# Kernel tuning notes

Measured on AMD Instinct MI355X. Metric: run time of the kernel, lower is better.

## Reference

```python
import jax, jax.numpy as jnp
import numpy as np


def setup_inputs() -> dict:
    key = jax.random.key(0)
    kq, kk, kv = jax.random.split(key, 3)
    B, H, S, D = 4, 16, 1024, 64
    Q = jax.random.normal(kq, (B, H, S, D), dtype=jnp.float32)
    K = jax.random.normal(kk, (B, H, S, D), dtype=jnp.float32)
    V = jax.random.normal(kv, (B, H, S, D), dtype=jnp.float32)
    attn_mask = jnp.ones((B, 1, 1, S), dtype=jnp.int32)  # unused by the original forward
    return {"Q": Q, "K": K, "V": V, "attn_mask": attn_mask, "d_k": D}


def reference(Q, K, V, attn_mask, d_k):
    # scores = Q @ K^T / sqrt(d_k)   -> [B, H, S, S]
    scores = jnp.einsum("bhqd,bhkd->bhqk", Q, K) / jnp.sqrt(jnp.float32(d_k))
    # attn_mask is accepted but never applied in the original module.
    p_attn = jax.nn.softmax(scores, axis=-1)
    out = jnp.einsum("bhqk,bhkd->bhqd", p_attn, V)  # [B, H, S, D]
    return (out, p_attn)
```

## Files before the change

### kernel.cpp

```cpp
#include <hip/hip_runtime.h>
#include <hip/hip_bf16.h>

#define B_N 4
#define H_N 16
#define S_N 1024
#define D_N 64
#define NELEM (B_N * H_N * S_N * D_N)

typedef __bf16 bf16;
typedef bf16  bf16x4 __attribute__((ext_vector_type(4)));
typedef bf16  bf16x8 __attribute__((ext_vector_type(8)));
typedef float f32x4  __attribute__((ext_vector_type(4)));
typedef unsigned int u32x2 __attribute__((ext_vector_type(2)));

#define AS1 __attribute__((address_space(1)))
#define AS3 __attribute__((address_space(3)))
#define GLL16(gp, lp) __builtin_amdgcn_global_load_lds((const AS1 void*)(gp), (AS3 void*)(lp), 16, 0, 0)

__global__ __launch_bounds__(256)
void prep_qk(const float* __restrict__ Q, const float* __restrict__ K,
             bf16* __restrict__ Qb, bf16* __restrict__ Kb)
{
    int t = blockIdx.x * 256 + threadIdx.x;
    const int half = NELEM / 8;
    bool isQ = t < half;
    int tt = isQ ? t : t - half;
    int row = tt >> 3, sub = tt & 7;
    const float* src = (isQ ? Q : K) + (size_t)row * 64 + sub * 8;
    float4 f0 = *(const float4*)src;
    float4 f1 = *(const float4*)(src + 4);
    float s = isQ ? 0.125f : 1.0f;
    bf16x8 o;
    o[0] = (bf16)(f0.x * s); o[1] = (bf16)(f0.y * s);
    o[2] = (bf16)(f0.z * s); o[3] = (bf16)(f0.w * s);
    o[4] = (bf16)(f1.x * s); o[5] = (bf16)(f1.y * s);
    o[6] = (bf16)(f1.z * s); o[7] = (bf16)(f1.w * s);
    int slot = isQ ? sub : (sub ^ (row & 7));
    bf16* dst = (isQ ? Qb : Kb) + (size_t)row * 64 + slot * 8;
    *(bf16x8*)dst = o;
}

__global__ __launch_bounds__(256)
void prep_v(const float* __restrict__ V, bf16* __restrict__ Vt)
{
    int wid  = blockIdx.x * 4 + (threadIdx.x >> 6);
    int lane = threadIdx.x & 63;
    int bh = wid >> 7, chunk = wid & 127;
    const float* src = V + (size_t)bh * S_N * D_N + (size_t)chunk * 8 * 64 + lane;
    bf16x8 o;
#pragma unroll
    for (int j = 0; j < 8; ++j) o[j] = (bf16)src[j * 64];
    int slot = (chunk & 7) ^ (lane & 7);
    bf16* dst = Vt + (size_t)bh * D_N * S_N + (size_t)lane * S_N
                   + (chunk >> 3) * 64 + slot * 8;
    *(bf16x8*)dst = o;
}

__global__ __launch_bounds__(256)
void sdpa_main(const bf16* __restrict__ Qb, const bf16* __restrict__ Kb,
               const bf16* __restrict__ Vt, float* __restrict__ Og,
               float* __restrict__ Pg)
{
    __shared__ __attribute__((aligned(128))) bf16 K_lds[2][4096];
    __shared__ __attribute__((aligned(128))) bf16 V_lds[2][4096];
    __shared__ __attribute__((aligned(128))) bf16 Pt_lds[4][1024];

    const int bid = blockIdx.x;
    const int swz = (bid & 7) * 128 + (bid >> 3);
    const int bh = swz >> 4, qtile = swz & 15;

    const int tid = threadIdx.x;
    const int wave = tid >> 6, lane = tid & 63;
    const int l16 = lane & 15, lgrp = lane >> 4;
    const int swx = (l16 & 7) << 4;

    const bf16* Qp = Qb + (size_t)bh * S_N * D_N;
    const bf16* Kp = Kb + (size_t)bh * S_N * D_N;
    const bf16* Vp = Vt + (size_t)bh * D_N * S_N;
    float* Op = Og + (size_t)bh * S_N * D_N;
    float* Pp = Pg + (size_t)bh * S_N * S_N;

    const int qrow = qtile * 64 + wave * 16 + l16;
    bf16x8 aq[2];
    aq[0] = *(const bf16x8*)(Qp + (size_t)qrow * 64 + lgrp * 8);
    aq[1] = *(const bf16x8*)(Qp + (size_t)qrow * 64 + 32 + lgrp * 8);

    auto stage_k = [&](int kt, int buf) {
        const bf16* gk = Kp + (size_t)kt * 64;
        GLL16(gk + (wave    ) * 512 + lane * 8, &K_lds[buf][(wave    ) * 512]);
        GLL16(gk + (wave + 4) * 512 + lane * 8, &K_lds[buf][(wave + 4) * 512]);
    };
    auto stage_v = [&](int kt, int buf) {
        const int dr = lane >> 3, c7 = lane & 7;
        GLL16(Vp + (size_t)((wave    ) * 8 + dr) * S_N + kt + c7 * 8, &V_lds[buf][(wave    ) * 512]);
        GLL16(Vp + (size_t)((wave + 4) * 8 + dr) * S_N + kt + c7 * 8, &V_lds[buf][(wave + 4) * 512]);
    };

    auto scores = [&](const bf16* base, f32x4 (&acc)[4]) {
#pragma unroll
        for (int kb = 0; kb < 4; ++kb) {
            acc[kb] = (f32x4){0.f, 0.f, 0.f, 0.f};
#pragma unroll
            for (int ds = 0; ds < 2; ++ds) {
                bf16x8 bk = *(const bf16x8*)((const char*)base
                            + (kb * 16 + l16) * 128
                            + ((ds * 64 + lgrp * 16) ^ swx));
                acc[kb] = __builtin_amdgcn_mfma_f32_16x16x32_bf16(aq[ds], bk, acc[kb], 0, 0, 0);
            }
        }
    };

    float lsum[4] = {0.f, 0.f, 0.f, 0.f};
    stage_k(0, 0);
    for (int t = 0; t < 16; ++t) {
        if (t < 15) {
            stage_k((t + 1) * 64, (t + 1) & 1);
            asm volatile("s_waitcnt vmcnt(2)" ::: "memory");
        } else {
            asm volatile("s_waitcnt vmcnt(0)" ::: "memory");
        }
        __builtin_amdgcn_s_barrier();
        f32x4 acc[4];
        scores(&K_lds[t & 1][0], acc);
#pragma unroll
        for (int kb = 0; kb < 4; ++kb)
#pragma unroll
            for (int r = 0; r < 4; ++r) lsum[r] += __expf(acc[kb][r]);
        __builtin_amdgcn_s_barrier();
    }
    float rl[4];
#pragma unroll
    for (int r = 0; r < 4; ++r) {
        float s = lsum[r];
        s += __shfl_xor(s, 1, 64);
        s += __shfl_xor(s, 2, 64);
        s += __shfl_xor(s, 4, 64);
        s += __shfl_xor(s, 8, 64);
        rl[r] = 1.0f / s;
    }

    f32x4 oacc[4];
#pragma unroll
    for (int db = 0; db < 4; ++db) oacc[db] = (f32x4){0.f, 0.f, 0.f, 0.f};

    const unsigned ptoff = (unsigned)(uintptr_t)(AS3 bf16*)(&Pt_lds[wave][0]);
    const int qg = qtile * 64 + wave * 16 + l16;

    stage_k(0, 0);
    stage_v(0, 0);
    for (int t = 0; t < 16; ++t) {
        const int kt = t * 64, buf = t & 1;
        if (t < 15) {
            stage_k(kt + 64, buf ^ 1);
            stage_v(kt + 64, buf ^ 1);
        }
        if (t == 0 || t == 15) asm volatile("s_waitcnt vmcnt(4)" ::: "memory");
        else                   asm volatile("s_waitcnt vmcnt(8)" ::: "memory");
        __builtin_amdgcn_s_barrier();

        f32x4 acc[4];
        scores(&K_lds[buf][0], acc);

#pragma unroll
        for (int kb = 0; kb < 4; ++kb) {
            bf16x4 pk;
#pragma unroll
            for (int r = 0; r < 4; ++r) pk[r] = (bf16)(__expf(acc[kb][r]) * rl[r]);
            *(bf16x4*)((char*)&Pt_lds[wave][0] + (kb * 16 + l16) * 32 + lgrp * 8) = pk;
        }
        asm volatile("s_waitcnt lgkmcnt(0)" ::: "memory");

        const bf16* vb = &V_lds[buf][0];
#pragma unroll
        for (int ks = 0; ks < 2; ++ks) {
            bf16x8 bv0 = *(const bf16x8*)((const char*)vb + (l16     ) * 128 + ((ks * 64 + lgrp * 16) ^ swx));
            bf16x8 bv1 = *(const bf16x8*)((const char*)vb + (16 + l16) * 128 + ((ks * 64 + lgrp * 16) ^ swx));
            bf16x8 bv2 = *(const bf16x8*)((const char*)vb + (32 + l16) * 128 + ((ks * 64 + lgrp * 16) ^ swx));
            bf16x8 bv3 = *(const bf16x8*)((const char*)vb + (48 + l16) * 128 + ((ks * 64 + lgrp * 16) ^ swx));

            u32x2 t0, t1;
            unsigned a = ptoff + ks * 1024 + lgrp * 256 + l16 * 8;
            asm volatile("ds_read_b64_tr_b16 %0, %2\n\t"
                         "ds_read_b64_tr_b16 %1, %2 offset:128"
                         : "=&v"(t0), "=&v"(t1) : "v"(a));
            asm volatile("s_waitcnt lgkmcnt(0)" ::: "memory");
            __builtin_amdgcn_sched_barrier(0);

            bf16x8 ap;
            ((unsigned*)&ap)[0] = t0[0]; ((unsigned*)&ap)[1] = t0[1];
            ((unsigned*)&ap)[2] = t1[0]; ((unsigned*)&ap)[3] = t1[1];

            float4 o0, o1;
            o0.x = __uint_as_float(t0[0] << 16);
            o0.y = __uint_as_float(t0[0] & 0xffff0000u);
            o0.z = __uint_as_float(t0[1] << 16);
            o0.w = __uint_as_float(t0[1] & 0xffff0000u);
            o1.x = __uint_as_float(t1[0] << 16);
            o1.y = __uint_as_float(t1[0] & 0xffff0000u);
            o1.z = __uint_as_float(t1[1] << 16);
            o1.w = __uint_as_float(t1[1] & 0xffff0000u);
            float* pp = Pp + (size_t)qg * S_N + kt + ks * 32 + lgrp * 8;
            *(float4*)pp = o0;
            *(float4*)(pp + 4) = o1;

            oacc[0] = __builtin_amdgcn_mfma_f32_16x16x32_bf16(ap, bv0, oacc[0], 0, 0, 0);
            oacc[1] = __builtin_amdgcn_mfma_f32_16x16x32_bf16(ap, bv1, oacc[1], 0, 0, 0);
            oacc[2] = __builtin_amdgcn_mfma_f32_16x16x32_bf16(ap, bv2, oacc[2], 0, 0, 0);
            oacc[3] = __builtin_amdgcn_mfma_f32_16x16x32_bf16(ap, bv3, oacc[3], 0, 0, 0);
        }
        __builtin_amdgcn_s_barrier();
    }

    const int qb0 = qtile * 64 + wave * 16 + lgrp * 4;
#pragma unroll
    for (int db = 0; db < 4; ++db)
#pragma unroll
        for (int r = 0; r < 4; ++r)
            Op[(size_t)(qb0 + r) * D_N + db * 16 + l16] = oacc[db][r];
}

__global__ __launch_bounds__(256)
void sdpa_fused(const float* __restrict__ Qg, const float* __restrict__ Kg,
                const float* __restrict__ Vg, float* __restrict__ Og,
                float* __restrict__ Pg)
{
    constexpr int LDP = 72;
    __shared__ bf16 K_lds [64][LDP];
    __shared__ bf16 Vt_lds[64][LDP];
    __shared__ bf16 P_lds [4][16][LDP];

    const int qtile = blockIdx.x;
    const int bh    = blockIdx.y;
    const int tid   = threadIdx.x;
    const int wave  = tid >> 6;
    const int lane  = tid & 63;
    const int l16   = lane & 15;
    const int lgrp  = lane >> 4;

    const float* Qp = Qg + (size_t)bh * S_N * D_N;
    const float* Kp = Kg + (size_t)bh * S_N * D_N;
    const float* Vp = Vg + (size_t)bh * S_N * D_N;
    float* Op = Og + (size_t)bh * S_N * D_N;
    float* Pp = Pg + (size_t)bh * S_N * S_N;

    const int qrow = qtile * 64 + wave * 16 + l16;
    bf16x8 aq[2];
#pragma unroll
    for (int ds = 0; ds < 2; ++ds) {
        const float* src = Qp + qrow * D_N + ds * 32 + lgrp * 8;
        float4 f0 = *(const float4*)(src);
        float4 f1 = *(const float4*)(src + 4);
        aq[ds][0] = (bf16)(f0.x * 0.125f); aq[ds][1] = (bf16)(f0.y * 0.125f);
        aq[ds][2] = (bf16)(f0.z * 0.125f); aq[ds][3] = (bf16)(f0.w * 0.125f);
        aq[ds][4] = (bf16)(f1.x * 0.125f); aq[ds][5] = (bf16)(f1.y * 0.125f);
        aq[ds][6] = (bf16)(f1.z * 0.125f); aq[ds][7] = (bf16)(f1.w * 0.125f);
    }

    auto stage_k = [&](int kt) {
#pragma unroll
        for (int i = 0; i < 4; ++i) {
            int slot = tid + i * 256;
            int row = slot >> 4, c4 = slot & 15;
            float4 f = *(const float4*)(Kp + (kt + row) * D_N + c4 * 4);
            bf16x4 pk = {(bf16)f.x, (bf16)f.y, (bf16)f.z, (bf16)f.w};
            *(bf16x4*)&K_lds[row][c4 * 4] = pk;
        }
    };
    auto stage_v = [&](int kt) {
#pragma unroll
        for (int i = 0; i < 4; ++i) {
            int slot = tid + i * 256;
            int row = slot >> 4, c4 = slot & 15;
            float4 f = *(const float4*)(Vp + (kt + row) * D_N + c4 * 4);
            Vt_lds[c4 * 4 + 0][row] = (bf16)f.x;
            Vt_lds[c4 * 4 + 1][row] = (bf16)f.y;
            Vt_lds[c4 * 4 + 2][row] = (bf16)f.z;
            Vt_lds[c4 * 4 + 3][row] = (bf16)f.w;
        }
    };
    auto compute_scores = [&](f32x4 (&acc)[4]) {
#pragma unroll
        for (int kb = 0; kb < 4; ++kb) {
            acc[kb] = (f32x4){0.f, 0.f, 0.f, 0.f};
#pragma unroll
            for (int ds = 0; ds < 2; ++ds) {
                bf16x8 bk = *(const bf16x8*)&K_lds[kb * 16 + l16][ds * 32 + lgrp * 8];
                acc[kb] = __builtin_amdgcn_mfma_f32_16x16x32_bf16(aq[ds], bk, acc[kb], 0, 0, 0);
            }
        }
    };

    float lsum[4] = {0.f, 0.f, 0.f, 0.f};
    for (int kt = 0; kt < S_N; kt += 64) {
        __syncthreads();
        stage_k(kt);
        __syncthreads();
        f32x4 acc[4];
        compute_scores(acc);
#pragma unroll
        for (int kb = 0; kb < 4; ++kb)
#pragma unroll
            for (int r = 0; r < 4; ++r) lsum[r] += __expf(acc[kb][r]);
    }
    float rl[4];
#pragma unroll
    for (int r = 0; r < 4; ++r) {
        float s = lsum[r];
        s += __shfl_xor(s, 1, 64);
        s += __shfl_xor(s, 2, 64);
        s += __shfl_xor(s, 4, 64);
        s += __shfl_xor(s, 8, 64);
        rl[r] = 1.0f / s;
    }

    f32x4 oacc[4];
#pragma unroll
    for (int db = 0; db < 4; ++db) oacc[db] = (f32x4){0.f, 0.f, 0.f, 0.f};
    const int qb0 = qtile * 64 + wave * 16 + lgrp * 4;

    for (int kt = 0; kt < S_N; kt += 64) {
        __syncthreads();
        stage_k(kt);
        stage_v(kt);
        __syncthreads();

        f32x4 acc[4];
        compute_scores(acc);
#pragma unroll
        for (int kb = 0; kb < 4; ++kb) {
#pragma unroll
            for (int r = 0; r < 4; ++r) {
                float p = __expf(acc[kb][r]) * rl[r];
                Pp[(size_t)(qb0 + r) * S_N + (kt + kb * 16 + l16)] = p;
                P_lds[wave][lgrp * 4 + r][kb * 16 + l16] = (bf16)p;
            }
        }
#pragma unroll
        for (int ks = 0; ks < 2; ++ks) {
            bf16x8 ap = *(const bf16x8*)&P_lds[wave][l16][ks * 32 + lgrp * 8];
#pragma unroll
            for (int db = 0; db < 4; ++db) {
                bf16x8 bv = *(const bf16x8*)&Vt_lds[db * 16 + l16][ks * 32 + lgrp * 8];
                oacc[db] = __builtin_amdgcn_mfma_f32_16x16x32_bf16(ap, bv, oacc[db], 0, 0, 0);
            }
        }
    }

#pragma unroll
    for (int db = 0; db < 4; ++db)
#pragma unroll
        for (int r = 0; r < 4; ++r)
            Op[(size_t)(qb0 + r) * D_N + db * 16 + l16] = oacc[db][r];
}

extern "C" void kernel_launch(void* const* d_in, const int* in_sizes, int n_in,
                              void* d_out, int out_size, void* d_ws, size_t ws_size,
                              hipStream_t stream) {
    const float* Q = (const float*)d_in[0];
    const float* K = (const float*)d_in[1];
    const float* V = (const float*)d_in[2];
    float* Out = (float*)d_out;
    float* P   = (float*)d_out + (size_t)NELEM;

    const size_t need = (size_t)NELEM * 2 * 3;
    if (ws_size >= need) {
        bf16* Qb = (bf16*)d_ws;
        bf16* Kb = Qb + NELEM;
        bf16* Vt = Kb + NELEM;
        prep_qk<<<dim3(2 * NELEM / 8 / 256), dim3(256), 0, stream>>>(Q, K, Qb, Kb);
        prep_v<<<dim3(64 * 128 / 4), dim3(256), 0, stream>>>(V, Vt);
        sdpa_main<<<dim3(1024), dim3(256), 0, stream>>>(Qb, Kb, Vt, Out, P);
    } else {
        sdpa_fused<<<dim3(16, 64), dim3(256), 0, stream>>>(Q, K, V, Out, P);
    }
}
```

Measured before the change: 105.1 us.

## Merge K/V prep kernels, convert Q in-kernel, reuse V LDS for wider K staging

Drops the separate Q bf16 conversion: the main kernel now loads fp32 Q rows, scales them and converts them into registers. The K and V prep kernels become a single launch. The first (row-sum) pass now processes 128 keys per step, borrowing the V LDS buffers as a second double buffer for K. The second pass issues the next tile's loads after the score MFMAs and uses __syncthreads instead of explicit vmcnt waits, which trades fine-grained overlap for simpler synchronization.

```diff
diff --git a/kernel.cpp b/kernel.cpp
--- a/kernel.cpp
+++ b/kernel.cpp
@@ -18,46 +18,38 @@
 #define GLL16(gp, lp) __builtin_amdgcn_global_load_lds((const AS1 void*)(gp), (AS3 void*)(lp), 16, 0, 0)
 
 __global__ __launch_bounds__(256)
-void prep_qk(const float* __restrict__ Q, const float* __restrict__ K,
-             bf16* __restrict__ Qb, bf16* __restrict__ Kb)
+void prep_kv(const float* __restrict__ K, const float* __restrict__ V,
+             bf16* __restrict__ Kb, bf16* __restrict__ Vt)
 {
-    int t = blockIdx.x * 256 + threadIdx.x;
-    const int half = NELEM / 8;
-    bool isQ = t < half;
-    int tt = isQ ? t : t - half;
-    int row = tt >> 3, sub = tt & 7;
-    const float* src = (isQ ? Q : K) + (size_t)row * 64 + sub * 8;
-    float4 f0 = *(const float4*)src;
-    float4 f1 = *(const float4*)(src + 4);
-    float s = isQ ? 0.125f : 1.0f;
-    bf16x8 o;
-    o[0] = (bf16)(f0.x * s); o[1] = (bf16)(f0.y * s);
-    o[2] = (bf16)(f0.z * s); o[3] = (bf16)(f0.w * s);
-    o[4] = (bf16)(f1.x * s); o[5] = (bf16)(f1.y * s);
-    o[6] = (bf16)(f1.z * s); o[7] = (bf16)(f1.w * s);
-    int slot = isQ ? sub : (sub ^ (row & 7));
-    bf16* dst = (isQ ? Qb : Kb) + (size_t)row * 64 + slot * 8;
-    *(bf16x8*)dst = o;
+    const int b = blockIdx.x;
+    if (b < 2048) {
+        int t = b * 256 + threadIdx.x;
+        int row = t >> 3, sub = t & 7;
+        const float* src = K + (size_t)row * 64 + sub * 8;
+        float4 f0 = *(const float4*)src;
+        float4 f1 = *(const float4*)(src + 4);
+        bf16x8 o;
+        o[0] = (bf16)f0.x; o[1] = (bf16)f0.y; o[2] = (bf16)f0.z; o[3] = (bf16)f0.w;
+        o[4] = (bf16)f1.x; o[5] = (bf16)f1.y; o[6] = (bf16)f1.z; o[7] = (bf16)f1.w;
+        int slot = sub ^ (row & 7);
+        *(bf16x8*)(Kb + (size_t)row * 64 + slot * 8) = o;
+    } else {
+        int wid  = (b - 2048) * 4 + (threadIdx.x >> 6);
+        int lane = threadIdx.x & 63;
+        int bh = wid >> 7, chunk = wid & 127;
+        const float* src = V + (size_t)bh * S_N * D_N + (size_t)chunk * 8 * 64 + lane;
+        bf16x8 o;
+#pragma unroll
+        for (int j = 0; j < 8; ++j) o[j] = (bf16)src[j * 64];
+        int slot = (chunk & 7) ^ (lane & 7);
+        bf16* dst = Vt + (size_t)bh * D_N * S_N + (size_t)lane * S_N
+                       + (chunk >> 3) * 64 + slot * 8;
+        *(bf16x8*)dst = o;
+    }
 }
 
 __global__ __launch_bounds__(256)
-void prep_v(const float* __restrict__ V, bf16* __restrict__ Vt)
-{
-    int wid  = blockIdx.x * 4 + (threadIdx.x >> 6);
-    int lane = threadIdx.x & 63;
-    int bh = wid >> 7, chunk = wid & 127;
-    const float* src = V + (size_t)bh * S_N * D_N + (size_t)chunk * 8 * 64 + lane;
-    bf16x8 o;
-#pragma unroll
-    for (int j = 0; j < 8; ++j) o[j] = (bf16)src[j * 64];
-    int slot = (chunk & 7) ^ (lane & 7);
-    bf16* dst = Vt + (size_t)bh * D_N * S_N + (size_t)lane * S_N
-                   + (chunk >> 3) * 64 + slot * 8;
-    *(bf16x8*)dst = o;
-}
-
-__global__ __launch_bounds__(256)
-void sdpa_main(const bf16* __restrict__ Qb, const bf16* __restrict__ Kb,
+void sdpa_main(const float* __restrict__ Qf, const bf16* __restrict__ Kb,
                const bf16* __restrict__ Vt, float* __restrict__ Og,
                float* __restrict__ Pg)
 {
@@ -74,7 +66,7 @@
     const int l16 = lane & 15, lgrp = lane >> 4;
     const int swx = (l16 & 7) << 4;
 
-    const bf16* Qp = Qb + (size_t)bh * S_N * D_N;
+    const float* Qp = Qf + (size_t)bh * S_N * D_N;
     const bf16* Kp = Kb + (size_t)bh * S_N * D_N;
     const bf16* Vp = Vt + (size_t)bh * D_N * S_N;
     float* Op = Og + (size_t)bh * S_N * D_N;
@@ -82,18 +74,33 @@
 
     const int qrow = qtile * 64 + wave * 16 + l16;
     bf16x8 aq[2];
-    aq[0] = *(const bf16x8*)(Qp + (size_t)qrow * 64 + lgrp * 8);
-    aq[1] = *(const bf16x8*)(Qp + (size_t)qrow * 64 + 32 + lgrp * 8);
-
-    auto stage_k = [&](int kt, int buf) {
+#pragma unroll
+    for (int ds = 0; ds < 2; ++ds) {
+        const float* src = Qp + (size_t)qrow * 64 + ds * 32 + lgrp * 8;
+        float4 f0 = *(const float4*)src;
+        float4 f1 = *(const float4*)(src + 4);
+        aq[ds][0] = (bf16)(f0.x * 0.125f); aq[ds][1] = (bf16)(f0.y * 0.125f);
+        aq[ds][2] = (bf16)(f0.z * 0.125f); aq[ds][3] = (bf16)(f0.w * 0.125f);
+        aq[ds][4] = (bf16)(f1.x * 0.125f); aq[ds][5] = (bf16)(f1.y * 0.125f);
+        aq[ds][6] = (bf16)(f1.z * 0.125f); aq[ds][7] = (bf16)(f1.w * 0.125f);
+    }
+
+    auto stage_k = [&](int kt, bf16* dst) {
         const bf16* gk = Kp + (size_t)kt * 64;
-        GLL16(gk + (wave    ) * 512 + lane * 8, &K_lds[buf][(wave    ) * 512]);
-        GLL16(gk + (wave + 4) * 512 + lane * 8, &K_lds[buf][(wave + 4) * 512]);
-    };
-    auto stage_v = [&](int kt, int buf) {
+        GLL16(gk + (wave    ) * 512 + lane * 8, dst + (wave    ) * 512);
+        GLL16(gk + (wave + 4) * 512 + lane * 8, dst + (wave + 4) * 512);
+    };
+    auto stage_k2 = [&](int kt, bf16* dst0, bf16* dst1) {
+        const bf16* gk = Kp + (size_t)kt * 64;
+        GLL16(gk + (wave     ) * 512 + lane * 8, dst0 + (wave    ) * 512);
+        GLL16(gk + (wave + 4 ) * 512 + lane * 8, dst0 + (wave + 4) * 512);
+        GLL16(gk + (wave + 8 ) * 512 + lane * 8, dst1 + (wave    ) * 512);
+        GLL16(gk + (wave + 12) * 512 + lane * 8, dst1 + (wave + 4) * 512);
+    };
+    auto stage_v = [&](int kt, bf16* dst) {
         const int dr = lane >> 3, c7 = lane & 7;
-        GLL16(Vp + (size_t)((wave    ) * 8 + dr) * S_N + kt + c7 * 8, &V_lds[buf][(wave    ) * 512]);
-        GLL16(Vp + (size_t)((wave + 4) * 8 + dr) * S_N + kt + c7 * 8, &V_lds[buf][(wave + 4) * 512]);
+        GLL16(Vp + (size_t)((wave    ) * 8 + dr) * S_N + kt + c7 * 8, dst + (wave    ) * 512);
+        GLL16(Vp + (size_t)((wave + 4) * 8 + dr) * S_N + kt + c7 * 8, dst + (wave + 4) * 512);
     };
 
     auto scores = [&](const bf16* base, f32x4 (&acc)[4]) {
@@ -111,22 +118,26 @@
     };
 
     float lsum[4] = {0.f, 0.f, 0.f, 0.f};
-    stage_k(0, 0);
-    for (int t = 0; t < 16; ++t) {
-        if (t < 15) {
-            stage_k((t + 1) * 64, (t + 1) & 1);
-            asm volatile("s_waitcnt vmcnt(2)" ::: "memory");
-        } else {
-            asm volatile("s_waitcnt vmcnt(0)" ::: "memory");
-        }
-        __builtin_amdgcn_s_barrier();
+    stage_k2(0, &K_lds[0][0], &K_lds[1][0]);
+    __syncthreads();
+    for (int c = 0; c < 8; ++c) {
+        const bf16* b0 = (c & 1) ? &V_lds[0][0] : &K_lds[0][0];
+        const bf16* b1 = (c & 1) ? &V_lds[1][0] : &K_lds[1][0];
+        bf16* n0 = (c & 1) ? &K_lds[0][0] : &V_lds[0][0];
+        bf16* n1 = (c & 1) ? &K_lds[1][0] : &V_lds[1][0];
+        if (c < 7) stage_k2((c + 1) * 128, n0, n1);
         f32x4 acc[4];
-        scores(&K_lds[t & 1][0], acc);
+        scores(b0, acc);
 #pragma unroll
         for (int kb = 0; kb < 4; ++kb)
 #pragma unroll
             for (int r = 0; r < 4; ++r) lsum[r] += __expf(acc[kb][r]);
-        __builtin_amdgcn_s_barrier();
+        scores(b1, acc);
+#pragma unroll
+        for (int kb = 0; kb < 4; ++kb)
+#pragma unroll
+            for (int r = 0; r < 4; ++r) lsum[r] += __expf(acc[kb][r]);
+        __syncthreads();
     }
     float rl[4];
 #pragma unroll
@@ -146,20 +157,19 @@
     const unsigned ptoff = (unsigned)(uintptr_t)(AS3 bf16*)(&Pt_lds[wave][0]);
     const int qg = qtile * 64 + wave * 16 + l16;
 
-    stage_k(0, 0);
-    stage_v(0, 0);
+    stage_k(0, &K_lds[0][0]);
+    stage_v(0, &V_lds[0][0]);
+    __syncthreads();
     for (int t = 0; t < 16; ++t) {
         const int kt = t * 64, buf = t & 1;
-        if (t < 15) {
-            stage_k(kt + 64, buf ^ 1);
-            stage_v(kt + 64, buf ^ 1);
-        }
-        if (t == 0 || t == 15) asm volatile("s_waitcnt vmcnt(4)" ::: "memory");
-        else                   asm volatile("s_waitcnt vmcnt(8)" ::: "memory");
-        __builtin_amdgcn_s_barrier();
 
         f32x4 acc[4];
         scores(&K_lds[buf][0], acc);
+
+        if (t < 15) {
+            stage_k(kt + 64, &K_lds[buf ^ 1][0]);
+            stage_v(kt + 64, &V_lds[buf ^ 1][0]);
+        }
 
 #pragma unroll
         for (int kb = 0; kb < 4; ++kb) {
@@ -208,7 +218,7 @@
             oacc[2] = __builtin_amdgcn_mfma_f32_16x16x32_bf16(ap, bv2, oacc[2], 0, 0, 0);
             oacc[3] = __builtin_amdgcn_mfma_f32_16x16x32_bf16(ap, bv3, oacc[3], 0, 0, 0);
         }
-        __builtin_amdgcn_s_barrier();
+        __syncthreads();
     }
 
     const int qb0 = qtile * 64 + wave * 16 + lgrp * 4;
@@ -362,14 +372,12 @@
     float* Out = (float*)d_out;
     float* P   = (float*)d_out + (size_t)NELEM;
 
-    const size_t need = (size_t)NELEM * 2 * 3;
+    const size_t need = (size_t)NELEM * 2 * 2;
     if (ws_size >= need) {
-        bf16* Qb = (bf16*)d_ws;
-        bf16* Kb = Qb + NELEM;
+        bf16* Kb = (bf16*)d_ws;
         bf16* Vt = Kb + NELEM;
-        prep_qk<<<dim3(2 * NELEM / 8 / 256), dim3(256), 0, stream>>>(Q, K, Qb, Kb);
-        prep_v<<<dim3(64 * 128 / 4), dim3(256), 0, stream>>>(V, Vt);
-        sdpa_main<<<dim3(1024), dim3(256), 0, stream>>>(Qb, Kb, Vt, Out, P);
+        prep_kv<<<dim3(4096), dim3(256), 0, stream>>>(K, V, Kb, Vt);
+        sdpa_main<<<dim3(1024), dim3(256), 0, stream>>>(Q, Kb, Vt, Out, P);
     } else {
         sdpa_fused<<<dim3(16, 64), dim3(256), 0, stream>>>(Q, K, V, Out, P);
     }
```

After: 96.24 us. 1.09x faster.
